# Performance work log

Measured on AMD Instinct MI355X. Metric: run time of the kernel, lower is better.

## Reference

```python
import jax, jax.numpy as jnp
import numpy as np

D_MODEL = 1024
N_HEADS = 16
HEAD_DIM = D_MODEL // N_HEADS
D_FF = 4096
BATCH = 4
SEQ = 2048
LN_EPS = 1e-5


def layer_norm(x, g, b):
    mu = jnp.mean(x, axis=-1, keepdims=True)
    var = jnp.mean(jnp.square(x - mu), axis=-1, keepdims=True)
    return (x - mu) * jax.lax.rsqrt(var + LN_EPS) * g + b


def setup_inputs() -> dict:
    key = jax.random.key(0)
    ks = jax.random.split(key, 8)
    s = 0.02
    x = jax.random.normal(ks[0], (BATCH, SEQ, D_MODEL), jnp.float32)
    mask = jnp.triu(jnp.ones((SEQ, SEQ), dtype=bool), k=1)  # True = masked
    return {
        "x": x,
        "ln1_g": jnp.ones((D_MODEL,), jnp.float32),
        "ln1_b": jnp.zeros((D_MODEL,), jnp.float32),
        "qkv_w": jax.random.normal(ks[1], (3 * D_MODEL, D_MODEL), jnp.float32) * s,
        "qkv_b": jnp.zeros((3 * D_MODEL,), jnp.float32),
        "out_w": jax.random.normal(ks[2], (D_MODEL, D_MODEL), jnp.float32) * s,
        "out_b": jnp.zeros((D_MODEL,), jnp.float32),
        "ln2_g": jnp.ones((D_MODEL,), jnp.float32),
        "ln2_b": jnp.zeros((D_MODEL,), jnp.float32),
        "fc1_w": jax.random.normal(ks[3], (D_FF, D_MODEL), jnp.float32) * s,
        "fc1_b": jnp.zeros((D_FF,), jnp.float32),
        "fc2_w": jax.random.normal(ks[4], (D_MODEL, D_FF), jnp.float32) * s,
        "fc2_b": jnp.zeros((D_MODEL,), jnp.float32),
        "mask": mask,
    }


def reference(x, ln1_g, ln1_b, qkv_w, qkv_b, out_w, out_b,
              ln2_g, ln2_b, fc1_w, fc1_b, fc2_w, fc2_b, mask):
    b, s, _ = x.shape
    # --- pre-norm attention ---
    h = layer_norm(x, ln1_g, ln1_b)
    qkv = h @ qkv_w.T + qkv_b                       # [b, s, 3*D]
    qkv = qkv.reshape(b, s, 3, N_HEADS, HEAD_DIM)
    q, k, v = (jnp.moveaxis(qkv[:, :, i], 2, 1) for i in range(3))  # [b, H, s, hd]
    scale = HEAD_DIM ** -0.5
    attn = jnp.einsum('bhqd,bhkd->bhqk', q, k) * scale
    attn = jnp.where(mask, -jnp.inf, attn)
    attn = jax.nn.softmax(attn, axis=-1)
    o = jnp.einsum('bhqk,bhkd->bhqd', attn, v)      # [b, H, s, hd]
    o = jnp.moveaxis(o, 1, 2).reshape(b, s, D_MODEL)
    x = x + (o @ out_w.T + out_b)
    # --- pre-norm FFN ---
    h = layer_norm(x, ln2_g, ln2_b)
    h = jax.nn.gelu(h @ fc1_w.T + fc1_b, approximate=False)
    x = x + (h @ fc2_w.T + fc2_b)
    return x
```

## Files before the change

### kernel.cpp

```cpp
#include <hip/hip_runtime.h>
#include <math.h>

using u16 = unsigned short;
typedef __attribute__((ext_vector_type(8))) short short8;
typedef __attribute__((ext_vector_type(4))) float f32x4;
typedef __attribute__((ext_vector_type(16))) float f32x16;
typedef __attribute__((ext_vector_type(4))) u16 u16x4;

#define DEV __device__ __forceinline__

DEV u16 f2bf(float f) {
    unsigned u = __float_as_uint(f);
    u += 0x7fffu + ((u >> 16) & 1u);
    return (u16)(u >> 16);
}
DEV float bf2f(u16 h) { return __uint_as_float(((unsigned)h) << 16); }

DEV short8 ld16(const u16* p) { return *reinterpret_cast<const short8*>(p); }

DEV float gelu_f(float x) { return 0.5f * x * (1.f + erff(x * 0.70710678118654752f)); }

DEV unsigned pk2(float a, float b) {
    unsigned r;
    asm("v_cvt_pk_bf16_f32 %0, %1, %2" : "=v"(r) : "v"(a), "v"(b));
    return r;
}

#define GLL16(gp, lp)                                                          \
    __builtin_amdgcn_global_load_lds(                                          \
        (const __attribute__((address_space(1))) void*)(gp),                   \
        (__attribute__((address_space(3))) void*)(lp), 16, 0, 0)

__global__ void cvt_f32_bf16(const float* __restrict__ in, u16* __restrict__ out, int n4) {
    int i = blockIdx.x * 256 + threadIdx.x;
    if (i >= n4) return;
    float4 v = reinterpret_cast<const float4*>(in)[i];
    u16x4 o;
    o.x = f2bf(v.x); o.y = f2bf(v.y); o.z = f2bf(v.z); o.w = f2bf(v.w);
    reinterpret_cast<u16x4*>(out)[i] = o;
}

__global__ __launch_bounds__(256) void ln_bf16(const float* __restrict__ x,
                                               const float* __restrict__ gm,
                                               const float* __restrict__ bt,
                                               u16* __restrict__ out) {
    const int row = blockIdx.x, tid = threadIdx.x;
    const float4 v = reinterpret_cast<const float4*>(x + (long)row * 1024)[tid];
    float s  = v.x + v.y + v.z + v.w;
    float sq = v.x * v.x + v.y * v.y + v.z * v.z + v.w * v.w;
#pragma unroll
    for (int off = 1; off <= 32; off <<= 1) {
        s  += __shfl_xor(s, off);
        sq += __shfl_xor(sq, off);
    }
    __shared__ float ss[4], ssq[4];
    const int wave = tid >> 6, lane = tid & 63;
    if (lane == 0) { ss[wave] = s; ssq[wave] = sq; }
    __syncthreads();
    s  = ss[0] + ss[1] + ss[2] + ss[3];
    sq = ssq[0] + ssq[1] + ssq[2] + ssq[3];
    const float mu   = s * (1.f / 1024.f);
    const float var  = sq * (1.f / 1024.f) - mu * mu;
    const float rstd = rsqrtf(var + 1e-5f);
    const float4 g4 = reinterpret_cast<const float4*>(gm)[tid];
    const float4 b4 = reinterpret_cast<const float4*>(bt)[tid];
    u16x4 o;
    o.x = f2bf((v.x - mu) * rstd * g4.x + b4.x);
    o.y = f2bf((v.y - mu) * rstd * g4.y + b4.y);
    o.z = f2bf((v.z - mu) * rstd * g4.z + b4.z);
    o.w = f2bf((v.w - mu) * rstd * g4.w + b4.w);
    reinterpret_cast<u16x4*>(out + (long)row * 1024)[tid] = o;
}

#define TS(c, r) ((c) * 128 + (((((r) >> 3) ^ ((c) & 15))) << 3) + ((r) & 7))

template <int EPI>
__global__ __launch_bounds__(256, 3) void gemm_bt(
    const u16* __restrict__ A, const u16* __restrict__ B,
    const float* __restrict__ bias, const float* res, float* outf,
    u16* __restrict__ outb, u16* __restrict__ Qb, u16* __restrict__ Kb,
    u16* __restrict__ Vtb, int M, int N, int K) {
    constexpr int SHSZ = (EPI == 3) ? 16384 : 8192;
    __shared__ u16 shpool[SHSZ];
    u16* As = shpool;
    u16* Bs = shpool + 4096;

    const int tid = threadIdx.x;
    const int wave = tid >> 6, lane = tid & 63;
    const int lo = lane & 15, g = lane >> 4;
    const int wr = wave >> 1, wc = wave & 1;

    const int nwg = gridDim.x, chunk = nwg >> 3;
    const int wgid = (blockIdx.x & 7) * chunk + (blockIdx.x >> 3);
    const int NB = N >> 7;
    const int bm = wgid / NB, bn = wgid % NB;
    const int row0 = bm * 128, col0 = bn * 128;

    const int lrow = lane >> 2;
    const int lg   = (lane & 3) ^ ((lane >> 3) & 3);
    const u16* Ag = A + (long)(row0 + wave * 16 + lrow) * K + lg * 8;
    const u16* Bg = B + (long)(col0 + wave * 16 + lrow) * K + lg * 8;
    u16* Al = As + wave * 512;
    u16* Bl = Bs + wave * 512;

    const int agp = g ^ ((lo >> 1) & 3);
    f32x4 acc[4][4] = {};

    for (int k0 = 0; k0 < K; k0 += 32) {
        GLL16(Ag, Al);
        GLL16(Ag + 64 * (long)K, Al + 2048);
        GLL16(Bg, Bl);
        GLL16(Bg + 64 * (long)K, Bl + 2048);
        Ag += 32; Bg += 32;
        __syncthreads();
        short8 af[4], bfr[4];
#pragma unroll
        for (int m = 0; m < 4; ++m)
            af[m] = ld16(&As[(wr * 64 + m * 16 + lo) * 32 + agp * 8]);
#pragma unroll
        for (int n = 0; n < 4; ++n)
            bfr[n] = ld16(&Bs[(wc * 64 + n * 16 + lo) * 32 + agp * 8]);
        __builtin_amdgcn_s_setprio(1);
#pragma unroll
        for (int m = 0; m < 4; ++m)
#pragma unroll
            for (int n = 0; n < 4; ++n)
                acc[m][n] = __builtin_amdgcn_mfma_f32_16x16x32_bf16(
                    bfr[n], af[m], acc[m][n], 0, 0, 0);
        __builtin_amdgcn_s_setprio(0);
        __syncthreads();
    }

    if constexpr (EPI == 3) {
        if (col0 >= 2048) {
#pragma unroll
            for (int n = 0; n < 4; ++n) {
                const int cb = wc * 64 + n * 16 + g * 4;
                const float4 b4 = *reinterpret_cast<const float4*>(&bias[col0 + cb]);
#pragma unroll
                for (int m = 0; m < 4; ++m) {
                    const int rl = wr * 64 + m * 16 + lo;
                    shpool[TS(cb + 0, rl)] = f2bf(acc[m][n][0] + b4.x);
                    shpool[TS(cb + 1, rl)] = f2bf(acc[m][n][1] + b4.y);
                    shpool[TS(cb + 2, rl)] = f2bf(acc[m][n][2] + b4.z);
                    shpool[TS(cb + 3, rl)] = f2bf(acc[m][n][3] + b4.w);
                }
            }
            __syncthreads();
            const int c = tid >> 1, half = tid & 1;
            const int dcol = (col0 - 2048) + c;
            const int head = dcol >> 6, d = dcol & 63;
            const int bb = row0 >> 11;
            u16* dst = Vtb + ((long)(bb * 16 + head) * 64 + d) * 2048 +
                       (row0 & 2047) + half * 64;
            const u16* srcb = shpool + c * 128;
#pragma unroll
            for (int i = 0; i < 8; ++i) {
                const int pc = (half * 8 + i) ^ (c & 15);
                *reinterpret_cast<short8*>(dst + i * 8) =
                    *reinterpret_cast<const short8*>(srcb + pc * 8);
            }
            return;
        }
    }
#pragma unroll
    for (int n = 0; n < 4; ++n) {
        const int cb = col0 + wc * 64 + n * 16 + g * 4;
        const float4 b4 = *reinterpret_cast<const float4*>(&bias[cb]);
#pragma unroll
        for (int m = 0; m < 4; ++m) {
            const int r = row0 + wr * 64 + m * 16 + lo;
            const float v0 = acc[m][n][0] + b4.x;
            const float v1 = acc[m][n][1] + b4.y;
            const float v2 = acc[m][n][2] + b4.z;
            const float v3 = acc[m][n][3] + b4.w;
            if constexpr (EPI == 0) {
                u16x4 o = {f2bf(v0), f2bf(v1), f2bf(v2), f2bf(v3)};
                *reinterpret_cast<u16x4*>(&outb[(long)r * N + cb]) = o;
            } else if constexpr (EPI == 1) {
                u16x4 o = {f2bf(gelu_f(v0)), f2bf(gelu_f(v1)),
                           f2bf(gelu_f(v2)), f2bf(gelu_f(v3))};
                *reinterpret_cast<u16x4*>(&outb[(long)r * N + cb]) = o;
            } else if constexpr (EPI == 2) {
                const float4 rr = *reinterpret_cast<const float4*>(&res[(long)r * N + cb]);
                float4 o = {rr.x + v0, rr.y + v1, rr.z + v2, rr.w + v3};
                *reinterpret_cast<float4*>(&outf[(long)r * N + cb]) = o;
            } else {
                const int part = cb >> 10, cc = cb & 1023;
                const int head = cc >> 6, d = cc & 63;
                const int bb = r >> 11, srow = r & 2047;
                const int bh = bb * 16 + head;
                u16x4 o = {f2bf(v0), f2bf(v1), f2bf(v2), f2bf(v3)};
                u16* base = (part == 0) ? Qb : Kb;
                *reinterpret_cast<u16x4*>(&base[((long)bh * 2048 + srow) * 64 + d]) = o;
            }
        }
    }
}

__global__ __launch_bounds__(256) void attn_fwd32(
    const u16* __restrict__ Q, const u16* __restrict__ K,
    const u16* __restrict__ Vt, u16* __restrict__ O) {
    const int bh = blockIdx.x;
    const int p = blockIdx.y;
    const int wave = threadIdx.x >> 6, lane = threadIdx.x & 63;
    const int lq = lane & 31, hi = lane >> 5;

    const u16* Kp = K + (long)bh * 2048 * 64;
    const u16* Vp = Vt + (long)bh * 64 * 2048;
    const int bb = bh >> 4, h = bh & 15;
    const float scale = 0.125f;

#pragma unroll
    for (int sp = 0; sp < 2; ++sp) {
        const int qt = sp ? p : (15 - p);
        const int qw = qt * 128 + wave * 32;
        const u16* Qp = Q + ((long)bh * 2048 + qw) * 64;

        short8 qf[4];
#pragma unroll
        for (int ks = 0; ks < 4; ++ks)
            qf[ks] = ld16(Qp + lq * 64 + ks * 16 + hi * 8);

        f32x16 o0 = {}, o1 = {};
        float m = -1e30f, l = 0.f;
        const int q_abs = qw + lq;
        const int nkv = qw + 32;

        for (int kv0 = 0; kv0 < nkv; kv0 += 64) {
            f32x16 s0 = {}, s1 = {};
            const u16* Kr = Kp + (long)(kv0 + lq) * 64 + hi * 8;
            __builtin_amdgcn_s_setprio(1);
#pragma unroll
            for (int ks = 0; ks < 4; ++ks)
                s0 = __builtin_amdgcn_mfma_f32_32x32x16_bf16(
                    ld16(Kr + ks * 16), qf[ks], s0, 0, 0, 0);
            const u16* Kr2 = Kr + 32 * 64;
#pragma unroll
            for (int ks = 0; ks < 4; ++ks)
                s1 = __builtin_amdgcn_mfma_f32_32x32x16_bf16(
                    ld16(Kr2 + ks * 16), qf[ks], s1, 0, 0, 0);
            __builtin_amdgcn_s_setprio(0);

            const u16* Vr = Vp + (long)lq * 2048 + kv0 + hi * 8;
            short8 vf0[4], vf1[4];
#pragma unroll
            for (int c = 0; c < 4; ++c) {
                vf0[c] = ld16(Vr + c * 16);
                vf1[c] = ld16(Vr + 32 * 2048 + c * 16);
            }

            float mt = -1e30f;
            if (kv0 + 64 >= nkv) {
#pragma unroll
                for (int r = 0; r < 16; ++r) {
                    const int kv = kv0 + (r & 3) + 8 * (r >> 2) + 4 * hi;
                    float v = s0[r] * scale;
                    if (kv > q_abs) v = -1e30f;
                    s0[r] = v; mt = fmaxf(mt, v);
                    v = s1[r] * scale;
                    if (kv + 32 > q_abs) v = -1e30f;
                    s1[r] = v; mt = fmaxf(mt, v);
                }
            } else {
#pragma unroll
                for (int r = 0; r < 16; ++r) {
                    s0[r] *= scale; s1[r] *= scale;
                    mt = fmaxf(mt, fmaxf(s0[r], s1[r]));
                }
            }
            mt = fmaxf(mt, __shfl_xor(mt, 32));

            if (!__all(mt <= m + 8.f)) {
                const float mn = fmaxf(m, mt);
                const float corr = __expf(m - mn);
                m = mn;
                l *= corr;
                o0 *= corr; o1 *= corr;
            }
            float ps = 0.f;
#pragma unroll
            for (int r = 0; r < 16; ++r) {
                s0[r] = __expf(s0[r] - m); ps += s0[r];
                s1[r] = __expf(s1[r] - m); ps += s1[r];
            }
            l += ps;

            short8 pf[4];
#pragma unroll
            for (int c = 0; c < 4; ++c) {
                const f32x16& src = (c >> 1) ? s1 : s0;
                const int b = (c & 1) * 8;
                const unsigned A0 = pk2(src[b + 0], src[b + 1]);
                const unsigned A1 = pk2(src[b + 2], src[b + 3]);
                const unsigned B0 = pk2(src[b + 4], src[b + 5]);
                const unsigned B1 = pk2(src[b + 6], src[b + 7]);
                const unsigned S0 = hi ? A0 : B0;
                const unsigned S1 = hi ? A1 : B1;
                const unsigned R0 = (unsigned)__shfl_xor((int)S0, 32);
                const unsigned R1 = (unsigned)__shfl_xor((int)S1, 32);
                union { unsigned u[4]; short8 v; } fr;
                fr.u[0] = hi ? R0 : A0;
                fr.u[1] = hi ? R1 : A1;
                fr.u[2] = hi ? B0 : R0;
                fr.u[3] = hi ? B1 : R1;
                pf[c] = fr.v;
            }

            __builtin_amdgcn_s_setprio(1);
#pragma unroll
            for (int c = 0; c < 4; ++c) {
                o0 = __builtin_amdgcn_mfma_f32_32x32x16_bf16(
                    vf0[c], pf[c], o0, 0, 0, 0);
                o1 = __builtin_amdgcn_mfma_f32_32x32x16_bf16(
                    vf1[c], pf[c], o1, 0, 0, 0);
            }
            __builtin_amdgcn_s_setprio(0);
        }

        l += __shfl_xor(l, 32);
        const float inv = 1.f / l;
        u16* Orow = O + ((long)(bb * 2048 + qw + lq)) * 1024 + h * 64;
#pragma unroll
        for (int k4 = 0; k4 < 4; ++k4) {
            u16x4 w0, w1;
#pragma unroll
            for (int j = 0; j < 4; ++j) {
                w0[j] = f2bf(o0[k4 * 4 + j] * inv);
                w1[j] = f2bf(o1[k4 * 4 + j] * inv);
            }
            *reinterpret_cast<u16x4*>(Orow + 8 * k4 + 4 * hi)      = w0;
            *reinterpret_cast<u16x4*>(Orow + 32 + 8 * k4 + 4 * hi) = w1;
        }
    }
}

extern "C" void kernel_launch(void* const* d_in, const int* in_sizes, int n_in,
                              void* d_out, int out_size, void* d_ws, size_t ws_size,
                              hipStream_t stream) {
    const float* x      = (const float*)d_in[0];
    const float* ln1_g  = (const float*)d_in[1];
    const float* ln1_b  = (const float*)d_in[2];
    const float* qkv_w  = (const float*)d_in[3];
    const float* qkv_b  = (const float*)d_in[4];
    const float* out_w  = (const float*)d_in[5];
    const float* out_b  = (const float*)d_in[6];
    const float* ln2_g  = (const float*)d_in[7];
    const float* ln2_b  = (const float*)d_in[8];
    const float* fc1_w  = (const float*)d_in[9];
    const float* fc1_b  = (const float*)d_in[10];
    const float* fc2_w  = (const float*)d_in[11];
    const float* fc2_b  = (const float*)d_in[12];
    float* out = (float*)d_out;

    const size_t MB = 1024ull * 1024ull;
    if (ws_size < 120 * MB) return;
    char* ws = (char*)d_ws;
    u16* wqkv = (u16*)(ws + 0);
    u16* wout = (u16*)(ws + 6 * MB);
    u16* wfc1 = (u16*)(ws + 8 * MB);
    u16* wfc2 = (u16*)(ws + 16 * MB);
    u16* hbuf = (u16*)(ws + 24 * MB);
    u16* obuf = (u16*)(ws + 40 * MB);
    u16* Qb   = (u16*)(ws + 56 * MB);
    u16* Kb   = (u16*)(ws + 72 * MB);
    u16* Vtb  = (u16*)(ws + 88 * MB);
    u16* gbuf = (u16*)(ws + 56 * MB);

    cvt_f32_bf16<<<3072, 256, 0, stream>>>(qkv_w, wqkv, 3072 * 1024 / 4);
    cvt_f32_bf16<<<1024, 256, 0, stream>>>(out_w, wout, 1024 * 1024 / 4);
    cvt_f32_bf16<<<4096, 256, 0, stream>>>(fc1_w, wfc1, 4096 * 1024 / 4);
    cvt_f32_bf16<<<4096, 256, 0, stream>>>(fc2_w, wfc2, 1024 * 4096 / 4);

    ln_bf16<<<8192, 256, 0, stream>>>(x, ln1_g, ln1_b, hbuf);
    gemm_bt<3><<<dim3(1536), 256, 0, stream>>>(hbuf, wqkv, qkv_b, nullptr,
                                               nullptr, nullptr, Qb, Kb, Vtb,
                                               8192, 3072, 1024);
    attn_fwd32<<<dim3(64, 8), 256, 0, stream>>>(Qb, Kb, Vtb, obuf);
    gemm_bt<2><<<dim3(512), 256, 0, stream>>>(obuf, wout, out_b, x, out,
                                              nullptr, nullptr, nullptr, nullptr,
                                              8192, 1024, 1024);
    ln_bf16<<<8192, 256, 0, stream>>>(out, ln2_g, ln2_b, hbuf);
    gemm_bt<1><<<dim3(2048), 256, 0, stream>>>(hbuf, wfc1, fc1_b, nullptr,
                                               nullptr, gbuf, nullptr, nullptr,
                                               nullptr, 8192, 4096, 1024);
    gemm_bt<2><<<dim3(512), 256, 0, stream>>>(gbuf, wfc2, fc2_b, out, out,
                                              nullptr, nullptr, nullptr, nullptr,
                                              8192, 1024, 4096);
}
```

Measured before the change: 452.8 us.

## Double-buffer GEMM LDS, fold softmax scale into Q, split attention grid

The GEMM mainloop now double-buffers LDS tiles: it issues global-to-LDS loads for the next K-step before computing the current one, so each iteration needs one barrier instead of two. The setprio calls around the GEMM MFMAs are removed. The QKV epilogue multiplies Q by scale*log2(e), which lets attention use exp2 directly without a per-score scale multiply, and the lazy-rescale threshold is adjusted to match. Attention no longer pairs two causal q-tiles per block; each block handles one tile on a 64x16 grid, which gives more blocks but relies on hardware scheduling to balance the uneven causal work.

```diff
diff --git a/kernel.cpp b/kernel.cpp
--- a/kernel.cpp
+++ b/kernel.cpp
@@ -80,10 +80,7 @@
     const float* __restrict__ bias, const float* res, float* outf,
     u16* __restrict__ outb, u16* __restrict__ Qb, u16* __restrict__ Kb,
     u16* __restrict__ Vtb, int M, int N, int K) {
-    constexpr int SHSZ = (EPI == 3) ? 16384 : 8192;
-    __shared__ u16 shpool[SHSZ];
-    u16* As = shpool;
-    u16* Bs = shpool + 4096;
+    __shared__ u16 shpool[16384];
 
     const int tid = threadIdx.x;
     const int wave = tid >> 6, lane = tid & 63;
@@ -100,19 +97,28 @@
     const int lg   = (lane & 3) ^ ((lane >> 3) & 3);
     const u16* Ag = A + (long)(row0 + wave * 16 + lrow) * K + lg * 8;
     const u16* Bg = B + (long)(col0 + wave * 16 + lrow) * K + lg * 8;
-    u16* Al = As + wave * 512;
-    u16* Bl = Bs + wave * 512;
+
+#define STAGE(tb, kt) do {                                                     \
+        u16* Al = shpool + (tb) * 8192 + wave * 512;                           \
+        u16* Bl = Al + 4096;                                                   \
+        GLL16(Ag + (long)(kt) * 32, Al);                                       \
+        GLL16(Ag + 64 * (long)K + (long)(kt) * 32, Al + 2048);                 \
+        GLL16(Bg + (long)(kt) * 32, Bl);                                       \
+        GLL16(Bg + 64 * (long)K + (long)(kt) * 32, Bl + 2048);                 \
+    } while (0)
 
     const int agp = g ^ ((lo >> 1) & 3);
     f32x4 acc[4][4] = {};
 
-    for (int k0 = 0; k0 < K; k0 += 32) {
-        GLL16(Ag, Al);
-        GLL16(Ag + 64 * (long)K, Al + 2048);
-        GLL16(Bg, Bl);
-        GLL16(Bg + 64 * (long)K, Bl + 2048);
-        Ag += 32; Bg += 32;
-        __syncthreads();
+    STAGE(0, 0);
+    __syncthreads();
+
+    const int T = K >> 5;
+    for (int t = 0; t < T; ++t) {
+        const int cur = t & 1;
+        if (t + 1 < T) STAGE(cur ^ 1, t + 1);
+        const u16* As = shpool + cur * 8192;
+        const u16* Bs = As + 4096;
         short8 af[4], bfr[4];
 #pragma unroll
         for (int m = 0; m < 4; ++m)
@@ -120,16 +126,15 @@
 #pragma unroll
         for (int n = 0; n < 4; ++n)
             bfr[n] = ld16(&Bs[(wc * 64 + n * 16 + lo) * 32 + agp * 8]);
-        __builtin_amdgcn_s_setprio(1);
 #pragma unroll
         for (int m = 0; m < 4; ++m)
 #pragma unroll
             for (int n = 0; n < 4; ++n)
                 acc[m][n] = __builtin_amdgcn_mfma_f32_16x16x32_bf16(
                     bfr[n], af[m], acc[m][n], 0, 0, 0);
-        __builtin_amdgcn_s_setprio(0);
         __syncthreads();
     }
+#undef STAGE
 
     if constexpr (EPI == 3) {
         if (col0 >= 2048) {
@@ -190,7 +195,8 @@
                 const int head = cc >> 6, d = cc & 63;
                 const int bb = r >> 11, srow = r & 2047;
                 const int bh = bb * 16 + head;
-                u16x4 o = {f2bf(v0), f2bf(v1), f2bf(v2), f2bf(v3)};
+                const float qs = (part == 0) ? 0.18033688f : 1.0f;
+                u16x4 o = {f2bf(v0 * qs), f2bf(v1 * qs), f2bf(v2 * qs), f2bf(v3 * qs)};
                 u16* base = (part == 0) ? Qb : Kb;
                 *reinterpret_cast<u16x4*>(&base[((long)bh * 2048 + srow) * 64 + d]) = o;
             }
@@ -202,136 +208,126 @@
     const u16* __restrict__ Q, const u16* __restrict__ K,
     const u16* __restrict__ Vt, u16* __restrict__ O) {
     const int bh = blockIdx.x;
-    const int p = blockIdx.y;
+    const int qt = 15 - blockIdx.y;
     const int wave = threadIdx.x >> 6, lane = threadIdx.x & 63;
     const int lq = lane & 31, hi = lane >> 5;
+    const int qw = qt * 128 + wave * 32;
 
     const u16* Kp = K + (long)bh * 2048 * 64;
     const u16* Vp = Vt + (long)bh * 64 * 2048;
     const int bb = bh >> 4, h = bh & 15;
-    const float scale = 0.125f;
-
-#pragma unroll
-    for (int sp = 0; sp < 2; ++sp) {
-        const int qt = sp ? p : (15 - p);
-        const int qw = qt * 128 + wave * 32;
-        const u16* Qp = Q + ((long)bh * 2048 + qw) * 64;
-
-        short8 qf[4];
+    const u16* Qp = Q + ((long)bh * 2048 + qw) * 64;
+
+    short8 qf[4];
+#pragma unroll
+    for (int ks = 0; ks < 4; ++ks)
+        qf[ks] = ld16(Qp + lq * 64 + ks * 16 + hi * 8);
+
+    f32x16 o0 = {}, o1 = {};
+    float m = -1e30f, l = 0.f;
+    const int q_abs = qw + lq;
+    const int nkv = qw + 32;
+
+    for (int kv0 = 0; kv0 < nkv; kv0 += 64) {
+        f32x16 s0 = {}, s1 = {};
+        const u16* Kr = Kp + (long)(kv0 + lq) * 64 + hi * 8;
+        __builtin_amdgcn_s_setprio(1);
 #pragma unroll
         for (int ks = 0; ks < 4; ++ks)
-            qf[ks] = ld16(Qp + lq * 64 + ks * 16 + hi * 8);
-
-        f32x16 o0 = {}, o1 = {};
-        float m = -1e30f, l = 0.f;
-        const int q_abs = qw + lq;
-        const int nkv = qw + 32;
-
-        for (int kv0 = 0; kv0 < nkv; kv0 += 64) {
-            f32x16 s0 = {}, s1 = {};
-            const u16* Kr = Kp + (long)(kv0 + lq) * 64 + hi * 8;
-            __builtin_amdgcn_s_setprio(1);
-#pragma unroll
-            for (int ks = 0; ks < 4; ++ks)
-                s0 = __builtin_amdgcn_mfma_f32_32x32x16_bf16(
-                    ld16(Kr + ks * 16), qf[ks], s0, 0, 0, 0);
-            const u16* Kr2 = Kr + 32 * 64;
-#pragma unroll
-            for (int ks = 0; ks < 4; ++ks)
-                s1 = __builtin_amdgcn_mfma_f32_32x32x16_bf16(
-                    ld16(Kr2 + ks * 16), qf[ks], s1, 0, 0, 0);
-            __builtin_amdgcn_s_setprio(0);
-
-            const u16* Vr = Vp + (long)lq * 2048 + kv0 + hi * 8;
-            short8 vf0[4], vf1[4];
-#pragma unroll
-            for (int c = 0; c < 4; ++c) {
-                vf0[c] = ld16(Vr + c * 16);
-                vf1[c] = ld16(Vr + 32 * 2048 + c * 16);
+            s0 = __builtin_amdgcn_mfma_f32_32x32x16_bf16(
+                ld16(Kr + ks * 16), qf[ks], s0, 0, 0, 0);
+        const u16* Kr2 = Kr + 32 * 64;
+#pragma unroll
+        for (int ks = 0; ks < 4; ++ks)
+            s1 = __builtin_amdgcn_mfma_f32_32x32x16_bf16(
+                ld16(Kr2 + ks * 16), qf[ks], s1, 0, 0, 0);
+        __builtin_amdgcn_s_setprio(0);
+
+        const u16* Vr = Vp + (long)lq * 2048 + kv0 + hi * 8;
+        short8 vf0[4], vf1[4];
+#pragma unroll
+        for (int c = 0; c < 4; ++c) {
+            vf0[c] = ld16(Vr + c * 16);
+            vf1[c] = ld16(Vr + 32 * 2048 + c * 16);
+        }
+
+        float mt = -1e30f;
+        if (kv0 + 64 >= nkv) {
+#pragma unroll
+            for (int r = 0; r < 16; ++r) {
+                const int kv = kv0 + (r & 3) + 8 * (r >> 2) + 4 * hi;
+                if (kv > q_abs) s0[r] = -1e30f;
+                mt = fmaxf(mt, s0[r]);
+                if (kv + 32 > q_abs) s1[r] = -1e30f;
+                mt = fmaxf(mt, s1[r]);
             }
-
-            float mt = -1e30f;
-            if (kv0 + 64 >= nkv) {
-#pragma unroll
-                for (int r = 0; r < 16; ++r) {
-                    const int kv = kv0 + (r & 3) + 8 * (r >> 2) + 4 * hi;
-                    float v = s0[r] * scale;
-                    if (kv > q_abs) v = -1e30f;
-                    s0[r] = v; mt = fmaxf(mt, v);
-                    v = s1[r] * scale;
-                    if (kv + 32 > q_abs) v = -1e30f;
-                    s1[r] = v; mt = fmaxf(mt, v);
-                }
-            } else {
-#pragma unroll
-                for (int r = 0; r < 16; ++r) {
-                    s0[r] *= scale; s1[r] *= scale;
-                    mt = fmaxf(mt, fmaxf(s0[r], s1[r]));
-                }
-            }
-            mt = fmaxf(mt, __shfl_xor(mt, 32));
-
-            if (!__all(mt <= m + 8.f)) {
-                const float mn = fmaxf(m, mt);
-                const float corr = __expf(m - mn);
-                m = mn;
-                l *= corr;
-                o0 *= corr; o1 *= corr;
-            }
-            float ps = 0.f;
-#pragma unroll
-            for (int r = 0; r < 16; ++r) {
-                s0[r] = __expf(s0[r] - m); ps += s0[r];
-                s1[r] = __expf(s1[r] - m); ps += s1[r];
-            }
-            l += ps;
-
-            short8 pf[4];
-#pragma unroll
-            for (int c = 0; c < 4; ++c) {
-                const f32x16& src = (c >> 1) ? s1 : s0;
-                const int b = (c & 1) * 8;
-                const unsigned A0 = pk2(src[b + 0], src[b + 1]);
-                const unsigned A1 = pk2(src[b + 2], src[b + 3]);
-                const unsigned B0 = pk2(src[b + 4], src[b + 5]);
-                const unsigned B1 = pk2(src[b + 6], src[b + 7]);
-                const unsigned S0 = hi ? A0 : B0;
-                const unsigned S1 = hi ? A1 : B1;
-                const unsigned R0 = (unsigned)__shfl_xor((int)S0, 32);
-                const unsigned R1 = (unsigned)__shfl_xor((int)S1, 32);
-                union { unsigned u[4]; short8 v; } fr;
-                fr.u[0] = hi ? R0 : A0;
-                fr.u[1] = hi ? R1 : A1;
-                fr.u[2] = hi ? B0 : R0;
-                fr.u[3] = hi ? B1 : R1;
-                pf[c] = fr.v;
-            }
-
-            __builtin_amdgcn_s_setprio(1);
-#pragma unroll
-            for (int c = 0; c < 4; ++c) {
-                o0 = __builtin_amdgcn_mfma_f32_32x32x16_bf16(
-                    vf0[c], pf[c], o0, 0, 0, 0);
-                o1 = __builtin_amdgcn_mfma_f32_32x32x16_bf16(
-                    vf1[c], pf[c], o1, 0, 0, 0);
-            }
-            __builtin_amdgcn_s_setprio(0);
-        }
-
-        l += __shfl_xor(l, 32);
-        const float inv = 1.f / l;
-        u16* Orow = O + ((long)(bb * 2048 + qw + lq)) * 1024 + h * 64;
-#pragma unroll
-        for (int k4 = 0; k4 < 4; ++k4) {
-            u16x4 w0, w1;
-#pragma unroll
-            for (int j = 0; j < 4; ++j) {
-                w0[j] = f2bf(o0[k4 * 4 + j] * inv);
-                w1[j] = f2bf(o1[k4 * 4 + j] * inv);
-            }
-            *reinterpret_cast<u16x4*>(Orow + 8 * k4 + 4 * hi)      = w0;
-            *reinterpret_cast<u16x4*>(Orow + 32 + 8 * k4 + 4 * hi) = w1;
-        }
+        } else {
+#pragma unroll
+            for (int r = 0; r < 16; ++r)
+                mt = fmaxf(mt, fmaxf(s0[r], s1[r]));
+        }
+        mt = fmaxf(mt, __shfl_xor(mt, 32));
+
+        if (!__all(mt <= m + 11.5f)) {
+            const float mn = fmaxf(m, mt);
+            const float corr = __builtin_amdgcn_exp2f(m - mn);
+            m = mn;
+            l *= corr;
+            o0 *= corr; o1 *= corr;
+        }
+        float ps = 0.f;
+#pragma unroll
+        for (int r = 0; r < 16; ++r) {
+            s0[r] = __builtin_amdgcn_exp2f(s0[r] - m); ps += s0[r];
+            s1[r] = __builtin_amdgcn_exp2f(s1[r] - m); ps += s1[r];
+        }
+        l += ps;
+
+        short8 pf[4];
+#pragma unroll
+        for (int c = 0; c < 4; ++c) {
+            const f32x16& src = (c >> 1) ? s1 : s0;
+            const int b = (c & 1) * 8;
+            const unsigned A0 = pk2(src[b + 0], src[b + 1]);
+            const unsigned A1 = pk2(src[b + 2], src[b + 3]);
+            const unsigned B0 = pk2(src[b + 4], src[b + 5]);
+            const unsigned B1 = pk2(src[b + 6], src[b + 7]);
+            const unsigned S0 = hi ? A0 : B0;
+            const unsigned S1 = hi ? A1 : B1;
+            const unsigned R0 = (unsigned)__shfl_xor((int)S0, 32);
+            const unsigned R1 = (unsigned)__shfl_xor((int)S1, 32);
+            union { unsigned u[4]; short8 v; } fr;
+            fr.u[0] = hi ? R0 : A0;
+            fr.u[1] = hi ? R1 : A1;
+            fr.u[2] = hi ? B0 : R0;
+            fr.u[3] = hi ? B1 : R1;
+            pf[c] = fr.v;
+        }
+
+        __builtin_amdgcn_s_setprio(1);
+#pragma unroll
+        for (int c = 0; c < 4; ++c) {
+            o0 = __builtin_amdgcn_mfma_f32_32x32x16_bf16(
+                vf0[c], pf[c], o0, 0, 0, 0);
+            o1 = __builtin_amdgcn_mfma_f32_32x32x16_bf16(
+                vf1[c], pf[c], o1, 0, 0, 0);
+        }
+        __builtin_amdgcn_s_setprio(0);
+    }
+
+    l += __shfl_xor(l, 32);
+    const float inv = 1.f / l;
+    u16* Orow = O + ((long)(bb * 2048 + qw + lq)) * 1024 + h * 64;
+#pragma unroll
+    for (int k4 = 0; k4 < 4; ++k4) {
+        u16x4 w0, w1;
+#pragma unroll
+        for (int j = 0; j < 4; ++j) {
+            w0[j] = f2bf(o0[k4 * 4 + j] * inv);
+            w1[j] = f2bf(o1[k4 * 4 + j] * inv);
+        }
+        *reinterpret_cast<u16x4*>(Orow + 8 * k4 + 4 * hi)      = w0;
+        *reinterpret_cast<u16x4*>(Orow + 32 + 8 * k4 + 4 * hi) = w1;
     }
 }
 
@@ -376,7 +372,7 @@
     gemm_bt<3><<<dim3(1536), 256, 0, stream>>>(hbuf, wqkv, qkv_b, nullptr,
                                                nullptr, nullptr, Qb, Kb, Vtb,
                                                8192, 3072, 1024);
-    attn_fwd32<<<dim3(64, 8), 256, 0, stream>>>(Qb, Kb, Vtb, obuf);
+    attn_fwd32<<<dim3(64, 16), 256, 0, stream>>>(Qb, Kb, Vtb, obuf);
     gemm_bt<2><<<dim3(512), 256, 0, stream>>>(obuf, wout, out_b, x, out,
                                               nullptr, nullptr, nullptr, nullptr,
                                               8192, 1024, 1024);
```

New measurement: 447.2 us. No clear change (-1.2%).
